# Kernel tuning notes

Hardware: AMD Instinct MI355X
Metric: run time of the kernel (lower is better)

Reference implementation:

```python
import jax, jax.numpy as jnp
import numpy as np

B, N, D = 256, 200000, 64
ACT_DIM, N_WP, N_ACT, H = 6, 512, 32, 64
SAME_WP_MIN = 8

def setup_inputs() -> dict:
    key = jax.random.key(0)
    ks = jax.random.split(key, 12)
    return {
        'q': jax.random.normal(ks[0], (B, D), jnp.float32),
        'library_vecs': jax.random.normal(ks[1], (N, D), jnp.float32),
        'retrieval_mask': jax.random.uniform(ks[2], (B, N)) < 0.1,
        'library_waypoint_ids': jax.random.randint(ks[3], (N,), 0, N_WP),
        'waypoint_id': jax.random.randint(ks[4], (B,), 0, N_WP),
        'action_id': jax.random.randint(ks[5], (B,), 0, N_ACT),
        'wp_action_prior': jax.random.uniform(ks[6], (B,), jnp.float32),
        'action_emb': jax.random.normal(ks[7], (N_ACT, ACT_DIM), jnp.float32) * 0.1,
        'W1': jax.random.normal(ks[8], (2 * D + ACT_DIM, H), jnp.float32) * (1.0 / np.sqrt(2 * D + ACT_DIM)),
        'b1': jnp.zeros((H,), jnp.float32),
        'W2': jax.random.normal(ks[9], (H, 1), jnp.float32) * (1.0 / np.sqrt(H)),
        'b2': jnp.zeros((1,), jnp.float32),
        'log_tau': jnp.asarray(np.log(0.5), jnp.float32),
        'prior_logit_weight': jnp.asarray(1.5, jnp.float32),
    }

def reference(q, library_vecs, retrieval_mask, library_waypoint_ids,
              waypoint_id, action_id, wp_action_prior, action_emb,
              W1, b1, W2, b2, log_tau, prior_logit_weight):
    NEG_INF = jnp.float32(-jnp.inf)
    tau = jnp.clip(jnp.exp(log_tau), 1e-3, 10.0)
    # [B, N] scores
    scores = jnp.einsum('bd,nd->bn', q, library_vecs) / tau
    scores = jnp.where(retrieval_mask, NEG_INF, scores)
    # same-waypoint hard filter
    wp_match = library_waypoint_ids[None, :] == waypoint_id[:, None]  # [B, N]
    valid_same_wp = wp_match & ~retrieval_mask
    same_wp_count = valid_same_wp.sum(axis=-1)
    sufficient = same_wp_count >= SAME_WP_MIN  # [B]
    wp_filter = (~wp_match) & sufficient[:, None]
    scores = jnp.where(wp_filter, NEG_INF, scores)
    attn = jax.nn.softmax(scores, axis=-1)  # [B, N]
    context = jnp.einsum('bn,nd->bd', attn, library_vecs)  # [B, D]
    action_vec = action_emb[action_id]  # [B, ACT_DIM]
    h = jnp.concatenate([q, context, action_vec], axis=-1)  # [B, 2D+ACT_DIM]
    h1 = jax.nn.gelu(h @ W1 + b1, approximate=False)
    logits = (h1 @ W2 + b2)[:, 0]  # [B]
    prior = jnp.clip(wp_action_prior, 1e-3, 1.0 - 1e-3)
    prior_logit = jnp.log(prior) - jnp.log1p(-prior)
    logits = logits + prior_logit_weight * prior_logit
    return logits, attn
```

## Files before the change

kernel.cpp:

```cpp
#include <hip/hip_runtime.h>
#include <cmath>

#define Nn 200000
#define Bq 256
#define NWP 512
#define NSEG 391
#define CAP 2048

__device__ __forceinline__ bool mask_at(const void* m, size_t idx, int isbyte) {
    if (isbyte) return ((const unsigned char*)m)[idx] != 0;
    return ((const unsigned int*)m)[idx] != 0u;
}

__global__ __launch_bounds__(512) void kc1d(const int* __restrict__ lib_wp,
                                            int* __restrict__ seg_cnt,
                                            const unsigned int* __restrict__ mw,
                                            int* __restrict__ flag) {
    __shared__ int hist[NWP];
    __shared__ int found;
    int t = threadIdx.x, seg = blockIdx.x;
    hist[t] = 0;
    if (t == 0) found = 0;
    __syncthreads();
    if (seg == 0) {
        int f = 0;
        for (int i = t; i < 4096; i += 512) {
            unsigned int w = mw[i];
            if (w >= 2u && w != 0x3F800000u) f = 1;
        }
        if (f) atomicOr(&found, 1);
    }
    int n = seg * 512 + t;
    if (n < Nn) {
        int w = lib_wp[n]; w = min(max(w, 0), NWP - 1);
        atomicAdd(&hist[w], 1);
    }
    __syncthreads();
    seg_cnt[seg * NWP + t] = hist[t];
    if (seg == 0 && t == 0) flag[0] = found;
}

__global__ __launch_bounds__(512) void kc2a_colscan(int* __restrict__ seg_cnt,
                                                    int* __restrict__ tot) {
    __shared__ int sc[512];
    int t = threadIdx.x, w = blockIdx.x;
    int v = (t < NSEG) ? seg_cnt[t * NWP + w] : 0;
    sc[t] = v;
    __syncthreads();
    for (int off = 1; off < 512; off <<= 1) {
        int x = (t >= off) ? sc[t - off] : 0;
        __syncthreads();
        sc[t] += x;
        __syncthreads();
    }
    if (t < NSEG)
        seg_cnt[t * NWP + w] = (t > 0) ? sc[t - 1] : 0;
    if (t == 0) tot[w] = sc[NSEG - 1];
}

__global__ __launch_bounds__(512) void kc2b_offscan(const int* __restrict__ tot,
                                                    int* __restrict__ offs) {
    __shared__ int sc[512];
    int t = threadIdx.x;
    sc[t] = tot[t];
    __syncthreads();
    for (int off = 1; off < 512; off <<= 1) {
        int x = (t >= off) ? sc[t - off] : 0;
        __syncthreads();
        sc[t] += x;
        __syncthreads();
    }
    offs[t] = (t > 0) ? sc[t - 1] : 0;
    if (t == 0) offs[NWP] = sc[NWP - 1];
}

__global__ __launch_bounds__(512) void kc3_scatter(const int* __restrict__ lib_wp,
                                                   const int* __restrict__ seg_cnt,
                                                   const int* __restrict__ offs,
                                                   int* __restrict__ bucket) {
    __shared__ int wps[512];
    int t = threadIdx.x, seg = blockIdx.x;
    int n = seg * 512 + t;
    int w = -1;
    if (n < Nn) { w = lib_wp[n]; w = min(max(w, 0), NWP - 1); }
    wps[t] = w;
    __syncthreads();
    if (n < Nn) {
        int r = 0;
        for (int j = 0; j < t; ++j) r += (wps[j] == w) ? 1 : 0;
        bucket[offs[w] + seg_cnt[seg * NWP + w] + r] = n;
    }
}

__global__ __launch_bounds__(256) void kA(
    const float* __restrict__ q, const float* __restrict__ lib, const void* __restrict__ mask,
    const int* __restrict__ wp_id, const int* __restrict__ offs, const int* __restrict__ bucket,
    const int* __restrict__ flag, const float* __restrict__ log_tau,
    float* __restrict__ attnbuf, float* __restrict__ pv, float* __restrict__ ctxws,
    int* __restrict__ suff, int* __restrict__ ovfl) {
    int bid = blockIdx.x;
    int t = threadIdx.x;
    int b = bid & 255;
    int slice = bid >> 8;
    if (slice > 0) {
        float4* rowp = (float4*)(attnbuf + (size_t)b * Nn + (size_t)(slice - 1) * 25000);
        const float4 z = make_float4(0.f, 0.f, 0.f, 0.f);
#pragma unroll 4
        for (int i = t; i < 6250; i += 256) rowp[i] = z;
        return;
    }
    __shared__ int   nlist[CAP];
    __shared__ unsigned char vbit[CAP];
    __shared__ float svals[CAP];
    __shared__ float ltile[64 * 65];
    __shared__ float q_s[64];
    __shared__ float red2[256];
    __shared__ int   redc[256];
    __shared__ float pbuf[64];
    __shared__ float Msh, Ssh, scale_sh;

    int isb = flag[0];
    int w = wp_id[b]; w = min(max(w, 0), NWP - 1);
    int off = offs[w], sz = offs[w + 1] - off;
    bool ov = sz > CAP;

    int c = 0;
    if (!ov) {
        for (int i = t; i < sz; i += 256) {
            int n = bucket[off + i];
            nlist[i] = n;
            bool vld = !mask_at(mask, (size_t)b * Nn + n, isb);
            vbit[i] = vld ? 1 : 0;
            c += vld ? 1 : 0;
        }
    } else {
        for (int i = t; i < sz; i += 256) {
            int n = bucket[off + i];
            c += mask_at(mask, (size_t)b * Nn + n, isb) ? 0 : 1;
        }
    }
    redc[t] = c;
    __syncthreads();
    for (int s2 = 128; s2 > 0; s2 >>= 1) {
        if (t < s2) redc[t] += redc[t + s2];
        __syncthreads();
    }
    int cnt = redc[0];
    bool sf = cnt >= 8;
    if (t == 0) { suff[b] = sf ? 1 : 0; ovfl[b] = ov ? 1 : 0; }
    if (!sf || ov) return;

    if (t < 64) q_s[t] = q[b * 64 + t];
    if (t == 0) { Msh = -INFINITY; Ssh = 0.f; }
    float tau = expf(log_tau[0]);
    tau = fminf(fmaxf(tau, 1e-3f), 10.0f);
    float inv_tau = 1.0f / tau;
    int d = t & 63, g = t >> 6;
    float ctxp = 0.f;
    __syncthreads();

    for (int c0 = 0; c0 < sz; c0 += 64) {
        int cn = min(64, sz - c0);
        int i = t >> 2, part = t & 3;
        if (i < cn) {
            int n_i = nlist[c0 + i];
            const float* src = &lib[(size_t)n_i * 64 + part * 16];
            float4 v0 = *(const float4*)&src[0];
            float4 v1 = *(const float4*)&src[4];
            float4 v2 = *(const float4*)&src[8];
            float4 v3 = *(const float4*)&src[12];
            float* dst = &ltile[i * 65 + part * 16];
            dst[0] = v0.x;  dst[1] = v0.y;  dst[2] = v0.z;  dst[3] = v0.w;
            dst[4] = v1.x;  dst[5] = v1.y;  dst[6] = v1.z;  dst[7] = v1.w;
            dst[8] = v2.x;  dst[9] = v2.y;  dst[10] = v2.z; dst[11] = v2.w;
            dst[12] = v3.x; dst[13] = v3.y; dst[14] = v3.z; dst[15] = v3.w;
        }
        __syncthreads();
        float s = -INFINITY;
        if (t < 64) {
            if (t < cn) {
                if (vbit[c0 + t]) {
                    float acc = 0.f;
#pragma unroll
                    for (int dd = 0; dd < 64; ++dd) acc = fmaf(q_s[dd], ltile[t * 65 + dd], acc);
                    s = acc * inv_tau;
                }
                svals[c0 + t] = s;
            }
            float m = s;
#pragma unroll
            for (int o = 1; o < 64; o <<= 1) m = fmaxf(m, __shfl_xor(m, o, 64));
            float e = (s > -INFINITY) ? expf(s - m) : 0.f;
#pragma unroll
            for (int o = 1; o < 64; o <<= 1) e += __shfl_xor(e, o, 64);
            if (t == 0) {
                float newM = fmaxf(Msh, m);
                if (newM > -INFINITY) {
                    float scl = expf(Msh - newM);
                    Ssh = Ssh * scl + e * expf(m - newM);
                    Msh = newM;
                    scale_sh = scl;
                } else {
                    scale_sh = 1.f;
                }
            }
        }
        __syncthreads();
        ctxp *= scale_sh;
        if (t < 64) pbuf[t] = (s > -INFINITY) ? expf(s - Msh) : 0.f;
        __syncthreads();
        for (int i2 = g; i2 < cn; i2 += 4)
            ctxp = fmaf(pbuf[i2], ltile[i2 * 65 + d], ctxp);
        __syncthreads();
    }
    float M = Msh, invS = 1.0f / Ssh;
    red2[t] = ctxp;
    __syncthreads();
    if (t < 64)
        ctxws[b * 64 + t] = (red2[t] + red2[64 + t] + red2[128 + t] + red2[192 + t]) * invS;
    for (int i = t; i < sz; i += 256) {
        float s2 = svals[i];
        pv[(size_t)b * CAP + i] = (s2 > -INFINITY) ? expf(s2 - M) * invS : 0.f;
    }
}

__global__ __launch_bounds__(256) void kB(
    const float* __restrict__ q, const float* __restrict__ lib, const void* __restrict__ mask,
    const int* __restrict__ lib_wp, const int* __restrict__ wp_id,
    const int* __restrict__ offs, const int* __restrict__ bucket,
    const int* __restrict__ flag, const int* __restrict__ suff, const int* __restrict__ ovfl,
    const float* __restrict__ log_tau, const float* __restrict__ pv,
    float* __restrict__ attnbuf, float* __restrict__ ctxws,
    const int* __restrict__ action_id, const float* __restrict__ act_emb,
    const float* __restrict__ W1, const float* __restrict__ b1,
    const float* __restrict__ W2, const float* __restrict__ b2,
    const float* __restrict__ wp_prior, const float* __restrict__ plw,
    float* __restrict__ out) {
    __shared__ float q_s[64];
    __shared__ float redm[4], reds[4];
    __shared__ float Msh, Ssh;
    __shared__ float pbuf2[256];
    int b = blockIdx.x, t = threadIdx.x;
    int sfb = suff[b], ov = ovfl[b];
    int w = wp_id[b]; w = min(max(w, 0), NWP - 1);

    if (sfb && !ov) {
        int off = offs[w], sz = offs[w + 1] - off;
        for (int i = t; i < sz; i += 256)
            attnbuf[(size_t)b * Nn + bucket[off + i]] = pv[(size_t)b * CAP + i];
    } else {
        if (t < 64) q_s[t] = q[b * 64 + t];
        if (t == 0) { Msh = -INFINITY; Ssh = 0.f; }
        int isb = flag[0];
        float tau = expf(log_tau[0]);
        tau = fminf(fmaxf(tau, 1e-3f), 10.0f);
        float inv_tau = 1.0f / tau;
        __syncthreads();
        for (int c0 = 0; c0 < Nn; c0 += 256) {
            int n = c0 + t;
            float s = -INFINITY;
            if (n < Nn) {
                bool mk = mask_at(mask, (size_t)b * Nn + n, isb);
                bool wpm = (lib_wp[n] == wp_id[b]);
                if (!mk && !(sfb && !wpm)) {
                    float acc = 0.f;
#pragma unroll
                    for (int dd = 0; dd < 64; dd += 4) {
                        float4 v = *(const float4*)&lib[(size_t)n * 64 + dd];
                        acc = fmaf(q_s[dd], v.x, acc);
                        acc = fmaf(q_s[dd + 1], v.y, acc);
                        acc = fmaf(q_s[dd + 2], v.z, acc);
                        acc = fmaf(q_s[dd + 3], v.w, acc);
                    }
                    s = acc * inv_tau;
                }
                attnbuf[(size_t)b * Nn + n] = s;
            }
            float m = s;
#pragma unroll
            for (int o = 1; o < 64; o <<= 1) m = fmaxf(m, __shfl_xor(m, o, 64));
            float e = (s > -INFINITY) ? expf(s - m) : 0.f;
#pragma unroll
            for (int o = 1; o < 64; o <<= 1) e += __shfl_xor(e, o, 64);
            if ((t & 63) == 0) { redm[t >> 6] = m; reds[t >> 6] = e; }
            __syncthreads();
            if (t == 0) {
                for (int wv = 0; wv < 4; ++wv) {
                    float m2 = redm[wv], e2 = reds[wv];
                    if (m2 > -INFINITY) {
                        if (m2 > Msh) { Ssh = Ssh * expf(Msh - m2) + e2; Msh = m2; }
                        else          { Ssh += e2 * expf(m2 - Msh); }
                    }
                }
            }
            __syncthreads();
        }
        float M = Msh, invS = 1.0f / Ssh;
        int d = t & 63, g = t >> 6;
        float ctxp = 0.f;
        for (int c0 = 0; c0 < Nn; c0 += 256) {
            int n = c0 + t;
            float p = 0.f;
            if (n < Nn) {
                float s = attnbuf[(size_t)b * Nn + n];
                p = (s > -INFINITY) ? expf(s - M) * invS : 0.f;
                attnbuf[(size_t)b * Nn + n] = p;
            }
            pbuf2[t] = p;
            __syncthreads();
            int lim = min(256, Nn - c0);
            for (int i2 = g; i2 < lim; i2 += 4) {
                float p2 = pbuf2[i2];
                if (p2 != 0.f) ctxp = fmaf(p2, lib[(size_t)(c0 + i2) * 64 + d], ctxp);
            }
            __syncthreads();
        }
        pbuf2[t] = ctxp;
        __syncthreads();
        if (t < 64)
            ctxws[b * 64 + t] = pbuf2[t] + pbuf2[64 + t] + pbuf2[128 + t] + pbuf2[192 + t];
    }
    __syncthreads();
    if (t < 64) {
        int j = t;
        float ctx = ctxws[b * 64 + j];
        float acc = b1[j];
        int aid = action_id[b];
        for (int i = 0; i < 64; ++i) acc = fmaf(q[b * 64 + i], W1[i * 64 + j], acc);
        for (int i = 0; i < 64; ++i) acc = fmaf(__shfl(ctx, i, 64), W1[(64 + i) * 64 + j], acc);
        for (int i = 0; i < 6; ++i) acc = fmaf(act_emb[aid * 6 + i], W1[(128 + i) * 64 + j], acc);
        float h1 = 0.5f * acc * (1.0f + erff(acc * 0.70710678118654752f));
        float v = h1 * W2[j];
#pragma unroll
        for (int o = 1; o < 64; o <<= 1) v += __shfl_xor(v, o, 64);
        if (j == 0) {
            float pr = fminf(fmaxf(wp_prior[b], 1e-3f), 1.0f - 1e-3f);
            float pl = logf(pr) - log1pf(-pr);
            out[b] = v + b2[0] + plw[0] * pl;
        }
    }
}

extern "C" void kernel_launch(void* const* d_in, const int* in_sizes, int n_in,
                              void* d_out, int out_size, void* d_ws, size_t ws_size,
                              hipStream_t stream) {
    const float* q = (const float*)d_in[0];
    const float* lib = (const float*)d_in[1];
    const void* mask = d_in[2];
    const int* lib_wp = (const int*)d_in[3];
    const int* wp_id = (const int*)d_in[4];
    const int* action_id = (const int*)d_in[5];
    const float* wp_prior = (const float*)d_in[6];
    const float* act_emb = (const float*)d_in[7];
    const float* W1 = (const float*)d_in[8];
    const float* b1 = (const float*)d_in[9];
    const float* W2 = (const float*)d_in[10];
    const float* b2 = (const float*)d_in[11];
    const float* log_tau = (const float*)d_in[12];
    const float* plw = (const float*)d_in[13];

    float* out = (float*)d_out;
    float* attnbuf = out + 256;

    char* ws = (char*)d_ws;
    int* flag    = (int*)(ws + 0);
    int* suff    = (int*)(ws + 1024);
    int* ovfl    = (int*)(ws + 2048);
    int* offs    = (int*)(ws + 4096);
    int* tot     = (int*)(ws + 8192);
    int* seg_cnt = (int*)(ws + 16384);
    int* bucket  = (int*)(ws + 851968);
    float* ctxws = (float*)(ws + 1703936);
    float* pv    = (float*)(ws + 2097152);

    kc1d<<<dim3(NSEG), 512, 0, stream>>>(lib_wp, seg_cnt, (const unsigned int*)mask, flag);
    kc2a_colscan<<<dim3(NWP), 512, 0, stream>>>(seg_cnt, tot);
    kc2b_offscan<<<1, 512, 0, stream>>>(tot, offs);
    kc3_scatter<<<dim3(NSEG), 512, 0, stream>>>(lib_wp, seg_cnt, offs, bucket);
    kA<<<dim3(9 * 256), 256, 0, stream>>>(q, lib, mask, wp_id, offs, bucket, flag, log_tau,
                                          attnbuf, pv, ctxws, suff, ovfl);
    kB<<<dim3(Bq), 256, 0, stream>>>(q, lib, mask, lib_wp, wp_id, offs, bucket, flag, suff,
                                     ovfl, log_tau, pv, attnbuf, ctxws, action_id, act_emb,
                                     W1, b1, W2, b2, wp_prior, plw, out);
}
```

Before: 79.84 us.

## Spread attn zero-fill across preprocessing kernels and fold offset scan into scatter

Splits the zeroing of the 256x200000 attention output into four quarters handled by extra blocks appended to the histogram, column-scan, scatter and kA launches, so the bandwidth-bound fill overlaps the small bucketing kernels. It also removes the single-block offset-scan kernel by having every scatter block recompute the 512-entry prefix sum in shared memory, cutting one launch. The cost is redundant scan work in each scatter block and extra blocks competing with the latency-sensitive preprocessing stages.

```diff
diff --git a/kernel.cpp b/kernel.cpp
--- a/kernel.cpp
+++ b/kernel.cpp
@@ -6,19 +6,34 @@
 #define NWP 512
 #define NSEG 391
 #define CAP 2048
+#define FILL_C 3200000
 
 __device__ __forceinline__ bool mask_at(const void* m, size_t idx, int isbyte) {
     if (isbyte) return ((const unsigned char*)m)[idx] != 0;
     return ((const unsigned int*)m)[idx] != 0u;
 }
 
+__device__ __forceinline__ void fillz(float4* __restrict__ p, int start4, int end4,
+                                      int fb, int nfb) {
+    int i = start4 + fb * blockDim.x + threadIdx.x;
+    int stride = nfb * blockDim.x;
+    const float4 z = make_float4(0.f, 0.f, 0.f, 0.f);
+    for (; i < end4; i += stride) p[i] = z;
+}
+
 __global__ __launch_bounds__(512) void kc1d(const int* __restrict__ lib_wp,
                                             int* __restrict__ seg_cnt,
                                             const unsigned int* __restrict__ mw,
-                                            int* __restrict__ flag) {
+                                            int* __restrict__ flag,
+                                            float4* __restrict__ fillp) {
+    int t = threadIdx.x, bid = blockIdx.x;
+    if (bid >= NSEG) {
+        fillz(fillp, 0, FILL_C, bid - NSEG, 512);
+        return;
+    }
     __shared__ int hist[NWP];
     __shared__ int found;
-    int t = threadIdx.x, seg = blockIdx.x;
+    int seg = bid;
     hist[t] = 0;
     if (t == 0) found = 0;
     __syncthreads();
@@ -41,9 +56,15 @@
 }
 
 __global__ __launch_bounds__(512) void kc2a_colscan(int* __restrict__ seg_cnt,
-                                                    int* __restrict__ tot) {
+                                                    int* __restrict__ tot,
+                                                    float4* __restrict__ fillp) {
+    int t = threadIdx.x, bid = blockIdx.x;
+    if (bid >= NWP) {
+        fillz(fillp, FILL_C, 2 * FILL_C, bid - NWP, 512);
+        return;
+    }
     __shared__ int sc[512];
-    int t = threadIdx.x, w = blockIdx.x;
+    int w = bid;
     int v = (t < NSEG) ? seg_cnt[t * NWP + w] : 0;
     sc[t] = v;
     __syncthreads();
@@ -58,10 +79,19 @@
     if (t == 0) tot[w] = sc[NSEG - 1];
 }
 
-__global__ __launch_bounds__(512) void kc2b_offscan(const int* __restrict__ tot,
-                                                    int* __restrict__ offs) {
+__global__ __launch_bounds__(512) void kc3_scatter(const int* __restrict__ lib_wp,
+                                                   const int* __restrict__ seg_cnt,
+                                                   const int* __restrict__ tot,
+                                                   int* __restrict__ offs_g,
+                                                   int* __restrict__ bucket,
+                                                   float4* __restrict__ fillp) {
+    int t = threadIdx.x, bid = blockIdx.x;
+    if (bid >= NSEG) {
+        fillz(fillp, 2 * FILL_C, 3 * FILL_C, bid - NSEG, 512);
+        return;
+    }
+    __shared__ int wps[512];
     __shared__ int sc[512];
-    int t = threadIdx.x;
     sc[t] = tot[t];
     __syncthreads();
     for (int off = 1; off < 512; off <<= 1) {
@@ -70,16 +100,11 @@
         sc[t] += x;
         __syncthreads();
     }
-    offs[t] = (t > 0) ? sc[t - 1] : 0;
-    if (t == 0) offs[NWP] = sc[NWP - 1];
-}
-
-__global__ __launch_bounds__(512) void kc3_scatter(const int* __restrict__ lib_wp,
-                                                   const int* __restrict__ seg_cnt,
-                                                   const int* __restrict__ offs,
-                                                   int* __restrict__ bucket) {
-    __shared__ int wps[512];
-    int t = threadIdx.x, seg = blockIdx.x;
+    if (bid == 0) {
+        offs_g[t] = (t > 0) ? sc[t - 1] : 0;
+        if (t == 0) offs_g[NWP] = sc[NWP - 1];
+    }
+    int seg = bid;
     int n = seg * 512 + t;
     int w = -1;
     if (n < Nn) { w = lib_wp[n]; w = min(max(w, 0), NWP - 1); }
@@ -88,7 +113,8 @@
     if (n < Nn) {
         int r = 0;
         for (int j = 0; j < t; ++j) r += (wps[j] == w) ? 1 : 0;
-        bucket[offs[w] + seg_cnt[seg * NWP + w] + r] = n;
+        int offw = (w > 0) ? sc[w - 1] : 0;
+        bucket[offw + seg_cnt[seg * NWP + w] + r] = n;
     }
 }
 
@@ -96,19 +122,15 @@
     const float* __restrict__ q, const float* __restrict__ lib, const void* __restrict__ mask,
     const int* __restrict__ wp_id, const int* __restrict__ offs, const int* __restrict__ bucket,
     const int* __restrict__ flag, const float* __restrict__ log_tau,
-    float* __restrict__ attnbuf, float* __restrict__ pv, float* __restrict__ ctxws,
+    float4* __restrict__ fillp, float* __restrict__ pv, float* __restrict__ ctxws,
     int* __restrict__ suff, int* __restrict__ ovfl) {
     int bid = blockIdx.x;
     int t = threadIdx.x;
-    int b = bid & 255;
-    int slice = bid >> 8;
-    if (slice > 0) {
-        float4* rowp = (float4*)(attnbuf + (size_t)b * Nn + (size_t)(slice - 1) * 25000);
-        const float4 z = make_float4(0.f, 0.f, 0.f, 0.f);
-#pragma unroll 4
-        for (int i = t; i < 6250; i += 256) rowp[i] = z;
+    if (bid >= 256) {
+        fillz(fillp, 3 * FILL_C, 4 * FILL_C, bid - 256, 1024);
         return;
     }
+    int b = bid;
     __shared__ int   nlist[CAP];
     __shared__ unsigned char vbit[CAP];
     __shared__ float svals[CAP];
@@ -361,6 +383,7 @@
 
     float* out = (float*)d_out;
     float* attnbuf = out + 256;
+    float4* fillp = (float4*)attnbuf;
 
     char* ws = (char*)d_ws;
     int* flag    = (int*)(ws + 0);
@@ -373,12 +396,13 @@
     float* ctxws = (float*)(ws + 1703936);
     float* pv    = (float*)(ws + 2097152);
 
-    kc1d<<<dim3(NSEG), 512, 0, stream>>>(lib_wp, seg_cnt, (const unsigned int*)mask, flag);
-    kc2a_colscan<<<dim3(NWP), 512, 0, stream>>>(seg_cnt, tot);
-    kc2b_offscan<<<1, 512, 0, stream>>>(tot, offs);
-    kc3_scatter<<<dim3(NSEG), 512, 0, stream>>>(lib_wp, seg_cnt, offs, bucket);
-    kA<<<dim3(9 * 256), 256, 0, stream>>>(q, lib, mask, wp_id, offs, bucket, flag, log_tau,
-                                          attnbuf, pv, ctxws, suff, ovfl);
+    kc1d<<<dim3(NSEG + 512), 512, 0, stream>>>(lib_wp, seg_cnt,
+                                               (const unsigned int*)mask, flag, fillp);
+    kc2a_colscan<<<dim3(NWP + 512), 512, 0, stream>>>(seg_cnt, tot, fillp);
+    kc3_scatter<<<dim3(NSEG + 512), 512, 0, stream>>>(lib_wp, seg_cnt, tot, offs, bucket,
+                                                      fillp);
+    kA<<<dim3(256 + 1024), 256, 0, stream>>>(q, lib, mask, wp_id, offs, bucket, flag,
+                                             log_tau, fillp, pv, ctxws, suff, ovfl);
     kB<<<dim3(Bq), 256, 0, stream>>>(q, lib, mask, lib_wp, wp_id, offs, bucket, flag, suff,
                                      ovfl, log_tau, pv, attnbuf, ctxws, action_id, act_emb,
                                      W1, b1, W2, b2, wp_prior, plw, out);
```

Result: no change. 80.59 us (+0.9%).
